# Kernel tuning notes

Measured on AMD Instinct MI355X. Metric: run time of the kernel, lower is better.

Reference implementation:

```python
import jax, jax.numpy as jnp
import numpy as np

B, H, K, T, OUT, NH = 512, 512, 6, 60, 2, 8

def _gelu(x):
    return jax.nn.gelu(x, approximate=False)  # torch nn.GELU default = exact erf

def _layernorm(x, g, b, eps=1e-5):
    m = jnp.mean(x, axis=-1, keepdims=True)
    v = jnp.var(x, axis=-1, keepdims=True)
    return (x - m) * jax.lax.rsqrt(v + eps) * g + b

def setup_inputs() -> dict:
    key = jax.random.key(0)
    ks = iter(jax.random.split(key, 40))
    def p(shape, scale=0.02):
        return jax.random.normal(next(ks), shape, dtype=jnp.float32) * scale
    return dict(
        interaction_ctx=p((B, H), 1.0),
        cooperative_ctx=p((B, H), 1.0),
        map_ctx=p((B, H), 1.0),
        mode_queries=p((K, H)),
        # context_proj: Linear(3H,H) -> GELU -> Linear(H,H)
        Wc1=p((3 * H, H)), bc1=jnp.zeros((H,), jnp.float32),
        Wc2=p((H, H)), bc2=jnp.zeros((H,), jnp.float32),
        # coarse_heads stacked over modes: Linear(H,2H)->GELU->Linear(2H,T*OUT)
        Wk1=p((K, H, 2 * H)), bk1=jnp.zeros((K, 2 * H), jnp.float32),
        Wk2=p((K, 2 * H, T * OUT)), bk2=jnp.zeros((K, T * OUT), jnp.float32),
        # traj_encoder: Linear(OUT,H)->GELU
        Wt=p((OUT, H)), bt=jnp.zeros((H,), jnp.float32),
        # refine_attn (MultiheadAttention) projections
        Wq_a=p((H, H)), bq_a=jnp.zeros((H,), jnp.float32),
        Wk_a=p((H, H)), bk_a=jnp.zeros((H,), jnp.float32),
        Wv_a=p((H, H)), bv_a=jnp.zeros((H,), jnp.float32),
        Wo_a=p((H, H)), bo_a=jnp.zeros((H,), jnp.float32),
        ln_g=jnp.ones((H,), jnp.float32), ln_b=jnp.zeros((H,), jnp.float32),
        # refine_heads stacked over modes: Linear(H,H)->GELU->Linear(H,OUT)
        Wr1=p((K, H, H)), br1=jnp.zeros((K, H), jnp.float32),
        Wr2=p((K, H, OUT)), br2=jnp.zeros((K, OUT), jnp.float32),
        # conf_head: Linear(H,64)->ReLU->Linear(64,1)
        Wf1=p((H, 64)), bf1=jnp.zeros((64,), jnp.float32),
        Wf2=p((64, 1)), bf2=jnp.zeros((1,), jnp.float32),
    )

def reference(interaction_ctx, cooperative_ctx, map_ctx, mode_queries,
              Wc1, bc1, Wc2, bc2, Wk1, bk1, Wk2, bk2, Wt, bt,
              Wq_a, bq_a, Wk_a, bk_a, Wv_a, bv_a, Wo_a, bo_a,
              ln_g, ln_b, Wr1, br1, Wr2, br2, Wf1, bf1, Wf2, bf2):
    # dropout layers are identity in eval mode
    combined = jnp.concatenate([interaction_ctx, cooperative_ctx, map_ctx], axis=-1)  # (B,3H)
    context = _gelu(combined @ Wc1 + bc1) @ Wc2 + bc2                                 # (B,H)
    mode_features = mode_queries[None, :, :] + context[:, None, :]                    # (B,K,H)

    # coarse heads: per-mode loop -> grouped GEMM over mode axis
    h = _gelu(jnp.einsum('bkh,khf->bkf', mode_features, Wk1) + bk1)                   # (B,K,2H)
    coarse = (jnp.einsum('bkf,kfo->bko', h, Wk2) + bk2).reshape(B, K, T, OUT)          # (B,K,T,OUT)

    traj_feats = _gelu(coarse @ Wt + bt)                                              # (B,K,T,H)

    # refine_attn: keys/values are context broadcast over T (all identical), so
    # softmax weights are exactly uniform and attention output == out_proj(v_ctx).
    # (grads through Wq_a/Wk_a are exactly zero for the same reason.)
    v = context @ Wv_a + bv_a                                                         # (B,H)
    attn_out = v @ Wo_a + bo_a                                                        # (B,H)

    refined_feats = _layernorm(traj_feats + attn_out[:, None, None, :], ln_g, ln_b)   # (B,K,T,H)

    # refine heads: grouped GEMM over mode axis
    r = _gelu(jnp.einsum('bkth,khf->bktf', refined_feats, Wr1) + br1[:, None, :])     # (B,K,T,H)
    offsets = jnp.einsum('bktf,kfo->bkto', r, Wr2) + br2[:, None, :]                  # (B,K,T,OUT)
    predictions = coarse + offsets

    conf = jax.nn.relu(mode_features @ Wf1 + bf1) @ Wf2 + bf2                         # (B,K,1)
    mode_probs = jax.nn.softmax(conf[..., 0], axis=-1)                                # (B,K)
    return predictions, mode_probs
```

## Files before the change

### kernel.cpp

```cpp
#include <hip/hip_runtime.h>
#include <math.h>

#define BB 512
#define HH 512
#define KK 6
#define TT 60
#define OO 2
#define H2 1024
#define TO 120
#define RFP 520
#define HSP 1032

typedef __bf16 bf16x8 __attribute__((ext_vector_type(8)));
typedef float  f32x4  __attribute__((ext_vector_type(4)));
typedef float  f32x16 __attribute__((ext_vector_type(16)));

__device__ __forceinline__ float bf2f(unsigned short u) {
    union { unsigned int i; float f; } v; v.i = ((unsigned int)u) << 16; return v.f;
}
__device__ __forceinline__ unsigned short f2bf(float f) {
    union { float f; unsigned int i; } v; v.f = f;
    unsigned int b = v.i;
    return (unsigned short)((b + 0x7FFFu + ((b >> 16) & 1u)) >> 16);
}
__device__ __forceinline__ unsigned int pack2bf(float a, float b) {
    union { __bf16 h[2]; unsigned int u; } v;
    v.h[0] = (__bf16)a; v.h[1] = (__bf16)b;
    return v.u;
}
__device__ __forceinline__ float gelu_exact(float x) {
    return 0.5f * x * (1.0f + erff(x * 0.70710678118654752f));
}

#if defined(__has_builtin)
#  if __has_builtin(__builtin_amdgcn_rcpf)
#    define FAST_RCP(x) __builtin_amdgcn_rcpf(x)
#  endif
#  if __has_builtin(__builtin_amdgcn_exp2f)
#    define FAST_EXP2(x) __builtin_amdgcn_exp2f(x)
#  endif
#endif
#ifndef FAST_RCP
#  define FAST_RCP(x) (1.0f / (x))
#endif
#ifndef FAST_EXP2
#  define FAST_EXP2(x) __expf((x) * 0.69314718056f)
#endif

__device__ __forceinline__ float gelu_cheap(float x) {
    float x2 = x * x;
    float z = x * fmaf(0.10294324f, x2, 2.3022082f);
    float e = FAST_EXP2(-z);
    return x * FAST_RCP(1.0f + e);
}

struct F8 { float v[8]; };
__device__ __forceinline__ F8 load8f(const float* p) {
    F8 r;
    float4 a = *(const float4*)p;
    float4 b = *(const float4*)(p + 4);
    r.v[0] = a.x; r.v[1] = a.y; r.v[2] = a.z; r.v[3] = a.w;
    r.v[4] = b.x; r.v[5] = b.y; r.v[6] = b.z; r.v[7] = b.w;
    return r;
}
__device__ __forceinline__ F8 load8b(const unsigned short* p) {
    ushort4 a = *(const ushort4*)p;
    ushort4 b = *(const ushort4*)(p + 4);
    F8 r;
    r.v[0] = bf2f(a.x); r.v[1] = bf2f(a.y); r.v[2] = bf2f(a.z); r.v[3] = bf2f(a.w);
    r.v[4] = bf2f(b.x); r.v[5] = bf2f(b.y); r.v[6] = bf2f(b.z); r.v[7] = bf2f(b.w);
    return r;
}

struct PKD { const float* src; unsigned short* dst; int F, N, NC, nch, steps, Z; };
struct PK8 { PKD e[8]; };

__global__ void k_pack(PK8 d) {
    int rid = blockIdx.x * 4 + (threadIdx.x >> 6);
    const int ln = threadIdx.x & 63;
    int i = 0;
    while (i < 7) {
        int tot = d.e[i].Z * d.e[i].nch * d.e[i].steps;
        if (rid < tot) break;
        rid -= tot; ++i;
    }
    const PKD e = d.e[i];
    const int per = e.nch * e.steps;
    const int z = rid / per;
    const int r = rid - z * per;
    const int nch = r / e.steps, step = r - nch * e.steps;
    const float* src = e.src + (size_t)z * e.F * e.N;
    unsigned short* dst = e.dst + ((size_t)z * per + r) * 512 + ln * 8;
    int f_base, n;
    if (e.NC == 16) { f_base = step * 32 + (ln >> 4) * 8; n = nch * 16 + (ln & 15); }
    else            { f_base = step * 16 + (ln >> 5) * 8; n = nch * 32 + (ln & 31); }
    if (n >= e.N) n = e.N - 1;
    unsigned int pk[4];
#pragma unroll
    for (int j = 0; j < 4; ++j) {
        unsigned short lo = f2bf(src[(size_t)(f_base + 2 * j) * e.N + n]);
        unsigned short hi = f2bf(src[(size_t)(f_base + 2 * j + 1) * e.N + n]);
        pk[j] = (unsigned int)lo | ((unsigned int)hi << 16);
    }
    *(uint4*)dst = make_uint4(pk[0], pk[1], pk[2], pk[3]);
}

template <bool CONCAT, bool GELU>
__launch_bounds__(256)
__global__ void k_gemm_m(const void* __restrict__ A0, const void* __restrict__ A1,
                         const void* __restrict__ A2, const unsigned short* __restrict__ BP,
                         const float* __restrict__ bias, unsigned short* __restrict__ C,
                         int Kd) {
    __shared__ __align__(16) unsigned short As[32 * RFP];
    const int tid = threadIdx.x;
    const int bm = blockIdx.x * 32;
    const int bn = blockIdx.y * 32;
    const int w = tid >> 6, ln = tid & 63;
    const int lane15 = ln & 15, quad = ln >> 4;
    const int mh = w >> 1;
    const int ng = w & 1;
    const int n = bn + ng * 16 + lane15;
    const int nchunks = Kd / HH;
    const int stepsTot = Kd / 32;
    const int nchB = blockIdx.y * 2 + ng;

    f32x4 acc0 = {0.f, 0.f, 0.f, 0.f};

    for (int kc = 0; kc < nchunks; ++kc) {
        {
            int r = tid >> 3, c0 = (tid & 7) * 64;
            unsigned short* dp = As + r * RFP + c0;
            if (CONCAT) {
                const float* src = (kc == 0) ? (const float*)A0
                                 : (kc == 1) ? (const float*)A1 : (const float*)A2;
                const float* sp = src + (bm + r) * HH + c0;
                for (int c = 0; c < 64; c += 8) {
                    F8 v = load8f(sp + c);
                    unsigned int pk[4];
#pragma unroll
                    for (int j = 0; j < 4; ++j)
                        pk[j] = pack2bf(v.v[2 * j], v.v[2 * j + 1]);
                    *(uint4*)(dp + c) = make_uint4(pk[0], pk[1], pk[2], pk[3]);
                }
            } else {
                const unsigned short* sp = (const unsigned short*)A0 + (bm + r) * HH + c0;
                for (int c = 0; c < 64; c += 8)
                    *(uint4*)(dp + c) = *(const uint4*)(sp + c);
            }
        }
        __syncthreads();
        const unsigned short* bp = BP + ((size_t)nchB * stepsTot + kc * 16) * 512 + ln * 8;
#pragma unroll
        for (int f0 = 0; f0 < HH; f0 += 32) {
            bf16x8 a0 = *(const bf16x8*)(As + (mh * 16 + lane15) * RFP + f0 + quad * 8);
            bf16x8 bf = *(const bf16x8*)(bp);
            bp += 512;
            acc0 = __builtin_amdgcn_mfma_f32_16x16x32_bf16(a0, bf, acc0, 0, 0, 0);
        }
        __syncthreads();
    }
    const float bb = bias[n];
#pragma unroll
    for (int reg = 0; reg < 4; ++reg) {
        float v0 = acc0[reg] + bb;
        if (GELU) v0 = gelu_exact(v0);
        C[(bm + mh * 16 + quad * 4 + reg) * HH + n] = f2bf(v0);
    }
}

__launch_bounds__(256)
__global__ void k_g1w(const float* __restrict__ I0, const float* __restrict__ I1,
                      const float* __restrict__ I2, const unsigned short* __restrict__ Wc1P,
                      const float* __restrict__ bc1, unsigned short* __restrict__ tmp,
                      const float* __restrict__ Wv, const unsigned short* __restrict__ WoP,
                      const float* __restrict__ WoF, const float* __restrict__ bv,
                      const float* __restrict__ bo,
                      unsigned short* __restrict__ wvop, float* __restrict__ bvo)
{
    __shared__ __align__(16) unsigned short As[32 * RFP];
    const int tid = threadIdx.x;
    const int w = tid >> 6, ln = tid & 63;
    const int lane15 = ln & 15, quad = ln >> 4;
    const int mh = w >> 1, ng = w & 1;

    if (blockIdx.x >= 256) {
        const int gbid = blockIdx.x - 256;
        const int bm = (gbid & 15) * 32;
        const int bn = (gbid >> 4) * 32;
        {
            int r = tid >> 3, c0 = (tid & 7) * 64;
            const float* sp = Wv + (size_t)(bm + r) * HH + c0;
            unsigned short* dp = As + r * RFP + c0;
            for (int c = 0; c < 64; c += 8) {
                F8 v = load8f(sp + c);
                unsigned int pk[4];
#pragma unroll
                for (int j = 0; j < 4; ++j)
                    pk[j] = pack2bf(v.v[2 * j], v.v[2 * j + 1]);
                *(uint4*)(dp + c) = make_uint4(pk[0], pk[1], pk[2], pk[3]);
            }
        }
        __syncthreads();
        const int n = bn + ng * 16 + lane15;
        const int nchB = (bn >> 4) + ng;
        f32x4 acc0 = {0.f, 0.f, 0.f, 0.f};
        const unsigned short* bp = WoP + (size_t)nchB * 16 * 512 + ln * 8;
#pragma unroll
        for (int f0 = 0; f0 < HH; f0 += 32) {
            bf16x8 a0 = *(const bf16x8*)(As + (mh * 16 + lane15) * RFP + f0 + quad * 8);
            bf16x8 bf = *(const bf16x8*)(bp);
            bp += 512;
            acc0 = __builtin_amdgcn_mfma_f32_16x16x32_bf16(a0, bf, acc0, 0, 0, 0);
        }
        const int step2 = bm >> 5;
        const int nch2 = n >> 4;
#pragma unroll
        for (int reg = 0; reg < 4; ++reg) {
            const int r5 = mh * 16 + quad * 4 + reg;
            const int ln2 = ((r5 >> 3) << 4) | lane15;
            wvop[((size_t)(nch2 * 16 + step2)) * 512 + ln2 * 8 + (r5 & 7)] = f2bf(acc0[reg]);
        }
        if (bm == 0 && w == 0 && ln < 32) {
            const int nn = bn + ln;
            float s = 0.f;
            for (int f = 0; f < HH; ++f) s = fmaf(bv[f], WoF[(size_t)f * HH + nn], s);
            bvo[nn] = s + bo[nn];
        }
        return;
    }

    const int bm = (blockIdx.x & 15) * 32;
    const int by = blockIdx.x >> 4;
    const int bn = by * 32;
    const int n = bn + ng * 16 + lane15;
    const int nchB = by * 2 + ng;
    const int stepsTot = 48;

    f32x4 acc0 = {0.f, 0.f, 0.f, 0.f};

    for (int kc = 0; kc < 3; ++kc) {
        {
            int r = tid >> 3, c0 = (tid & 7) * 64;
            unsigned short* dp = As + r * RFP + c0;
            const float* src = (kc == 0) ? I0 : (kc == 1) ? I1 : I2;
            const float* sp = src + (size_t)(bm + r) * HH + c0;
            for (int c = 0; c < 64; c += 8) {
                F8 v = load8f(sp + c);
                unsigned int pk[4];
#pragma unroll
                for (int j = 0; j < 4; ++j)
                    pk[j] = pack2bf(v.v[2 * j], v.v[2 * j + 1]);
                *(uint4*)(dp + c) = make_uint4(pk[0], pk[1], pk[2], pk[3]);
            }
        }
        __syncthreads();
        const unsigned short* bp = Wc1P + ((size_t)nchB * stepsTot + kc * 16) * 512 + ln * 8;
#pragma unroll
        for (int f0 = 0; f0 < HH; f0 += 32) {
            bf16x8 a0 = *(const bf16x8*)(As + (mh * 16 + lane15) * RFP + f0 + quad * 8);
            bf16x8 bf = *(const bf16x8*)(bp);
            bp += 512;
            acc0 = __builtin_amdgcn_mfma_f32_16x16x32_bf16(a0, bf, acc0, 0, 0, 0);
        }
        __syncthreads();
    }
    const float bb = bc1[n];
#pragma unroll
    for (int reg = 0; reg < 4; ++reg)
        tmp[(bm + mh * 16 + quad * 4 + reg) * HH + n] = f2bf(gelu_exact(acc0[reg] + bb));
}

__launch_bounds__(512)
__global__ void k_bcg(const unsigned short* __restrict__ ctx, const float* __restrict__ mq,
                      const unsigned short* __restrict__ Wk1P, const float* __restrict__ bk1,
                      const unsigned short* __restrict__ Wk2P, const float* __restrict__ bk2,
                      const unsigned short* __restrict__ Wf1P, const float* __restrict__ bf1,
                      const float* __restrict__ Wf2, const float* __restrict__ bf2v,
                      unsigned short* __restrict__ coarse_out, float* __restrict__ conf_out,
                      const unsigned short* __restrict__ WvoP, const float* __restrict__ bvo,
                      unsigned short* __restrict__ attn_out)
{
    __shared__ __align__(16) unsigned short shbuf[24832];

    const int tid = threadIdx.x;
    const int w = tid >> 6;
    const int ln = tid & 63;
    const int lane15 = ln & 15;
    const int quad = ln >> 4;

    if (blockIdx.x >= 192) {
        unsigned short* As = shbuf;
        const int gbid = blockIdx.x - 192;
        const int bm = (gbid & 15) * 32;
        const int gy = gbid >> 4;
        const int bn = gy * 64;
        const int mh = w >> 2;
        const int ng = w & 3;
        const int n = bn + ng * 16 + lane15;
        const int nchB = gy * 4 + ng;

        {
            int r = tid >> 4, c0 = (tid & 15) * 32;
            const unsigned short* sp = ctx + (bm + r) * HH + c0;
            unsigned short* dp = As + r * RFP + c0;
            for (int c = 0; c < 32; c += 8)
                *(uint4*)(dp + c) = *(const uint4*)(sp + c);
        }
        __syncthreads();
        f32x4 acc0 = {0.f, 0.f, 0.f, 0.f};
        const unsigned short* bp = WvoP + (size_t)nchB * 16 * 512 + ln * 8;
#pragma unroll
        for (int f0 = 0; f0 < HH; f0 += 32) {
            bf16x8 a0 = *(const bf16x8*)(As + (mh * 16 + lane15) * RFP + f0 + quad * 8);
            bf16x8 bf = *(const bf16x8*)(bp);
            bp += 512;
            acc0 = __builtin_amdgcn_mfma_f32_16x16x32_bf16(a0, bf, acc0, 0, 0, 0);
        }
        const float bb = bvo[n];
#pragma unroll
        for (int reg = 0; reg < 4; ++reg)
            attn_out[(bm + mh * 16 + quad * 4 + reg) * HH + n] = f2bf(acc0[reg] + bb);
        return;
    }

    unsigned short* mf = shbuf;
    unsigned short* hs = shbuf + 16 * RFP;
    const int k = blockIdx.x % KK;
    const int b0 = (blockIdx.x / KK) * 16;

    {
        int r = tid >> 5;
        int c0 = (tid & 31) * 16;
        const unsigned short* cp = ctx + (b0 + r) * HH + c0;
        const float* qp = mq + k * HH + c0;
        unsigned short* dp = mf + r * RFP + c0;
        for (int c = 0; c < 16; c += 8) {
            F8 cv = load8b(cp + c);
            F8 qv = load8f(qp + c);
            unsigned int pk[4];
#pragma unroll
            for (int j = 0; j < 4; ++j)
                pk[j] = pack2bf(cv.v[2 * j] + qv.v[2 * j], cv.v[2 * j + 1] + qv.v[2 * j + 1]);
            *(uint4*)(dp + c) = make_uint4(pk[0], pk[1], pk[2], pk[3]);
        }
    }
    __syncthreads();

    {
        const unsigned short* wk1p = Wk1P + (size_t)k * (64 * 16 * 512);
        const float* bk1p = bk1 + k * H2;
        for (int g = 0; g < 8; ++g) {
            const int n = w * 128 + g * 16 + lane15;
            f32x4 acc0 = {0.f,0.f,0.f,0.f};
            const unsigned short* bp = wk1p + (size_t)((w * 8 + g) * 16) * 512 + ln * 8;
#pragma unroll
            for (int f0 = 0; f0 < HH; f0 += 32) {
                bf16x8 a0 = *(const bf16x8*)(mf + lane15 * RFP + f0 + quad * 8);
                bf16x8 bf = *(const bf16x8*)(bp);
                bp += 512;
                acc0 = __builtin_amdgcn_mfma_f32_16x16x32_bf16(a0, bf, acc0, 0, 0, 0);
            }
            const float bias = bk1p[n];
#pragma unroll
            for (int reg = 0; reg < 4; ++reg)
                hs[(quad * 4 + reg) * HSP + n] = f2bf(gelu_exact(acc0[reg] + bias));
        }
    }
    __syncthreads();

    {
        const unsigned short* wk2p = Wk2P + (size_t)k * (8 * 32 * 512);
        const int n = w * 16 + lane15;
        f32x4 acc0 = {0.f,0.f,0.f,0.f};
        const unsigned short* bp = wk2p + (size_t)(w * 32) * 512 + ln * 8;
#pragma unroll
        for (int f0 = 0; f0 < H2; f0 += 32) {
            bf16x8 a0 = *(const bf16x8*)(hs + lane15 * HSP + f0 + quad * 8);
            bf16x8 bf = *(const bf16x8*)(bp);
            bp += 512;
            acc0 = __builtin_amdgcn_mfma_f32_16x16x32_bf16(a0, bf, acc0, 0, 0, 0);
        }
        if (n < TO) {
            const float bias = bk2[k * TO + n];
#pragma unroll
            for (int reg = 0; reg < 4; ++reg)
                coarse_out[((b0 + quad * 4 + reg) * KK + k) * TO + n] = f2bf(acc0[reg] + bias);
        }
    }

    if (w == 0) {
        f32x4 acc[4];
#pragma unroll
        for (int nt = 0; nt < 4; ++nt) { f32x4 z = {0.f,0.f,0.f,0.f}; acc[nt] = z; }
#pragma unroll
        for (int f0 = 0; f0 < HH; f0 += 32) {
            const int step = f0 >> 5;
            bf16x8 a0 = *(const bf16x8*)(mf + lane15 * RFP + f0 + quad * 8);
#pragma unroll
            for (int nt = 0; nt < 4; ++nt) {
                bf16x8 bf = *(const bf16x8*)(Wf1P + (size_t)(nt * 16 + step) * 512 + ln * 8);
                acc[nt] = __builtin_amdgcn_mfma_f32_16x16x32_bf16(a0, bf, acc[nt], 0, 0, 0);
            }
        }
        const float b2 = bf2v[0];
#pragma unroll
        for (int reg = 0; reg < 4; ++reg) {
            float s = 0.f;
#pragma unroll
            for (int nt = 0; nt < 4; ++nt) {
                const int n = nt * 16 + lane15;
                s = fmaf(fmaxf(acc[nt][reg] + bf1[n], 0.f), Wf2[n], s);
            }
#pragma unroll
            for (int off = 1; off < 16; off <<= 1) s += __shfl_xor(s, off);
            if (lane15 == 0)
                conf_out[(b0 + quad * 4 + reg) * KK + k] = s + b2;
        }
    }
}

__launch_bounds__(512, 4)
__global__ void k_ef(
    const unsigned short* __restrict__ attn, const unsigned short* __restrict__ coarse_ws,
    const float* __restrict__ Wt,  const float* __restrict__ bt,
    const float* __restrict__ lng, const float* __restrict__ lnb,
    const unsigned short* __restrict__ Wr1P, const float* __restrict__ br1,
    const float* __restrict__ Wr2, const float* __restrict__ br2,
    float* __restrict__ pred_out,
    const float* __restrict__ conf, float* __restrict__ probs)
{
    __shared__ __align__(16) unsigned short rf[64 * RFP];
    __shared__ float coarse[TO];
    __shared__ float br1s[HH];
    __shared__ float2 wr2s[HH];
    __shared__ float po2[8][64][2];

    const int tid = threadIdx.x;
    const int b = blockIdx.x / KK;
    const int k = blockIdx.x % KK;
    const int w = tid >> 6;
    const int ln = tid & 63;
    const int lane31 = ln & 31;
    const int hf = ln >> 5;
    const int cbase = ln * 8;

    const unsigned short* attb = attn + b * HH;

    if (tid < TO) coarse[tid] = bf2f(coarse_ws[(b * KK + k) * TO + tid]);
    br1s[tid] = br1[k * HH + tid];
    wr2s[tid] = ((const float2*)Wr2)[(size_t)k * HH + tid];

    if (k == 0 && tid == 448) {
        float v[KK]; float m = -1e30f;
#pragma unroll
        for (int i = 0; i < KK; ++i) { v[i] = conf[b * KK + i]; m = fmaxf(m, v[i]); }
        float s = 0.f;
#pragma unroll
        for (int i = 0; i < KK; ++i) { v[i] = __expf(v[i] - m); s += v[i]; }
        float inv = 1.0f / s;
#pragma unroll
        for (int i = 0; i < KK; ++i) probs[b * KK + i] = v[i] * inv;
    }
    __syncthreads();

    {
        F8 w0 = load8f(Wt + cbase);
        F8 w1 = load8f(Wt + HH + cbase);
        F8 b8 = load8f(bt + cbase);
        F8 g8 = load8f(lng + cbase);
        F8 bb8 = load8f(lnb + cbase);
        F8 a8 = load8b(attb + cbase);
#pragma unroll
        for (int g = 0; g < 2; ++g) {
            float x[4][8];
            float s[4], s2[4];
#pragma unroll
            for (int r = 0; r < 4; ++r) {
                const int t = w + 8 * (g * 4 + r);
                float ss = 0.f, ss2 = 0.f;
                if (t < 60) {
                    const float co0 = coarse[2 * t], co1 = coarse[2 * t + 1];
#pragma unroll
                    for (int j = 0; j < 8; ++j) {
                        float vv = fmaf(co0, w0.v[j], fmaf(co1, w1.v[j], b8.v[j]));
                        vv = gelu_cheap(vv) + a8.v[j];
                        x[r][j] = vv; ss += vv; ss2 = fmaf(vv, vv, ss2);
                    }
                } else {
#pragma unroll
                    for (int j = 0; j < 8; ++j) x[r][j] = 0.f;
                }
                s[r] = ss; s2[r] = ss2;
            }
#pragma unroll
            for (int off = 32; off > 0; off >>= 1) {
#pragma unroll
                for (int r = 0; r < 4; ++r) {
                    s[r] += __shfl_xor(s[r], off);
                    s2[r] += __shfl_xor(s2[r], off);
                }
            }
#pragma unroll
            for (int r = 0; r < 4; ++r) {
                const int t = w + 8 * (g * 4 + r);
                if (t < 60) {
                    float mean = s[r] * (1.0f / HH);
                    float var = fmaf(-mean, mean, s2[r] * (1.0f / HH));
                    float inv = rsqrtf(var + 1e-5f);
                    unsigned int pk[4];
#pragma unroll
                    for (int j = 0; j < 4; ++j) {
                        float y0 = fmaf((x[r][2 * j] - mean) * inv, g8.v[2 * j], bb8.v[2 * j]);
                        float y1 = fmaf((x[r][2 * j + 1] - mean) * inv, g8.v[2 * j + 1], bb8.v[2 * j + 1]);
                        pk[j] = pack2bf(y0, y1);
                    }
                    *(uint4*)(rf + t * RFP + cbase) = make_uint4(pk[0], pk[1], pk[2], pk[3]);
                } else {
                    *(uint4*)(rf + t * RFP + cbase) = make_uint4(0, 0, 0, 0);
                }
            }
        }
    }
    __syncthreads();

    {
        const unsigned short* bp0 = Wr1P + (size_t)k * (16 * 32 * 512)
                                  + (size_t)(w * 2) * 32 * 512 + ln * 8;
        const unsigned short* bp1 = bp0 + 32 * 512;
        const int n0 = w * 64;
        const unsigned short* a0p = rf + lane31 * RFP + hf * 8;
        const unsigned short* a1p = a0p + 32 * RFP;

        f32x16 acc00 = {0.f,0.f,0.f,0.f,0.f,0.f,0.f,0.f,0.f,0.f,0.f,0.f,0.f,0.f,0.f,0.f};
        f32x16 acc01 = acc00, acc10 = acc00, acc11 = acc00;

        __builtin_amdgcn_s_setprio(1);
#pragma unroll
        for (int st = 0; st < 32; ++st) {
            const int k0 = st * 16;
            bf16x8 A0 = *(const bf16x8*)(a0p + k0);
            bf16x8 A1 = *(const bf16x8*)(a1p + k0);
            bf16x8 B0 = *(const bf16x8*)(bp0 + st * 512);
            bf16x8 B1 = *(const bf16x8*)(bp1 + st * 512);
            acc00 = __builtin_amdgcn_mfma_f32_32x32x16_bf16(B0, A0, acc00, 0, 0, 0);
            acc01 = __builtin_amdgcn_mfma_f32_32x32x16_bf16(B1, A0, acc01, 0, 0, 0);
            acc10 = __builtin_amdgcn_mfma_f32_32x32x16_bf16(B0, A1, acc10, 0, 0, 0);
            acc11 = __builtin_amdgcn_mfma_f32_32x32x16_bf16(B1, A1, acc11, 0, 0, 0);
        }
        __builtin_amdgcn_s_setprio(0);

        float p00 = 0.f, p01 = 0.f, p10 = 0.f, p11 = 0.f;
#pragma unroll
        for (int nt = 0; nt < 2; ++nt) {
#pragma unroll
            for (int reg = 0; reg < 16; ++reg) {
                const int n = n0 + nt * 32 + (reg & 3) + 8 * (reg >> 2) + 4 * hf;
                const float bb = br1s[n];
                const float2 w2 = wr2s[n];
                const float a0v = nt ? acc01[reg] : acc00[reg];
                const float a1v = nt ? acc11[reg] : acc10[reg];
                const float rv0 = gelu_cheap(a0v + bb);
                const float rv1 = gelu_cheap(a1v + bb);
                p00 = fmaf(rv0, w2.x, p00);
                p01 = fmaf(rv0, w2.y, p01);
                p10 = fmaf(rv1, w2.x, p10);
                p11 = fmaf(rv1, w2.y, p11);
            }
        }
        p00 += __shfl_xor(p00, 32);
        p01 += __shfl_xor(p01, 32);
        p10 += __shfl_xor(p10, 32);
        p11 += __shfl_xor(p11, 32);
        if (ln < 32) {
            *(float2*)&po2[w][lane31][0]      = make_float2(p00, p01);
            *(float2*)&po2[w][32 + lane31][0] = make_float2(p10, p11);
        }
    }
    __syncthreads();

    if (tid < TO) {
        int t = tid >> 1, o = tid & 1;
        float s = 0.f;
#pragma unroll
        for (int ww = 0; ww < 8; ++ww) s += po2[ww][t][o];
        pred_out[((b * KK + k) * TT + t) * 2 + o] = coarse[tid] + s + br2[k * 2 + o];
    }
}

extern "C" void kernel_launch(void* const* d_in, const int* in_sizes, int n_in,
                              void* d_out, int out_size, void* d_ws, size_t ws_size,
                              hipStream_t stream) {
    const float* I0  = (const float*)d_in[0];
    const float* I1  = (const float*)d_in[1];
    const float* I2  = (const float*)d_in[2];
    const float* MQ  = (const float*)d_in[3];
    const float* Wc1 = (const float*)d_in[4];
    const float* bc1 = (const float*)d_in[5];
    const float* Wc2 = (const float*)d_in[6];
    const float* bc2 = (const float*)d_in[7];
    const float* Wk1 = (const float*)d_in[8];
    const float* bk1 = (const float*)d_in[9];
    const float* Wk2 = (const float*)d_in[10];
    const float* bk2 = (const float*)d_in[11];
    const float* Wt  = (const float*)d_in[12];
    const float* bt  = (const float*)d_in[13];
    const float* Wv  = (const float*)d_in[18];
    const float* bv  = (const float*)d_in[19];
    const float* Wo  = (const float*)d_in[20];
    const float* bo  = (const float*)d_in[21];
    const float* lng = (const float*)d_in[22];
    const float* lnb = (const float*)d_in[23];
    const float* Wr1 = (const float*)d_in[24];
    const float* br1 = (const float*)d_in[25];
    const float* Wr2 = (const float*)d_in[26];
    const float* br2 = (const float*)d_in[27];
    const float* Wf1 = (const float*)d_in[28];
    const float* bf1 = (const float*)d_in[29];
    const float* Wf2 = (const float*)d_in[30];
    const float* bf2v = (const float*)d_in[31];

    unsigned short* wsu   = (unsigned short*)d_ws;
    unsigned short* wc1p  = wsu;
    unsigned short* wc2p  = wsu + 786432;
    unsigned short* wvop  = wsu + 1048576;
    unsigned short* wop   = wsu + 1310720;
    unsigned short* wk1p  = wsu + 1572864;
    unsigned short* wk2p  = wsu + 4718592;
    unsigned short* wf1p  = wsu + 5505024;
    unsigned short* wr1p  = wsu + 5537792;
    unsigned short* ctx   = wsu + 7110656;
    unsigned short* attn  = wsu + 7372800;
    unsigned short* tmp   = wsu + 7634944;
    unsigned short* coarse= wsu + 7897088;
    float* conf = (float*)(wsu + 8265728);
    float* bvo  = (float*)(wsu + 8271872);

    float* pred = (float*)d_out;
    float* probs = pred + BB * KK * TT * OO;

    PK8 pk;
    pk.e[0] = {Wc1, wc1p, 3 * HH, HH, 16, 32, 48, 1};
    pk.e[1] = {Wc2, wc2p, HH, HH, 16, 32, 16, 1};
    pk.e[2] = {Wc2, wc2p, HH, HH, 16, 0, 16, 1};
    pk.e[3] = {Wo,  wop,  HH, HH, 16, 32, 16, 1};
    pk.e[4] = {Wk1, wk1p, HH, H2, 16, 64, 16, KK};
    pk.e[5] = {Wk2, wk2p, H2, TO, 16, 8, 32, KK};
    pk.e[6] = {Wf1, wf1p, HH, 64, 16, 4, 16, 1};
    pk.e[7] = {Wr1, wr1p, HH, HH, 32, 16, 32, KK};
    k_pack<<<dim3(3344), 256, 0, stream>>>(pk);

    k_g1w<<<dim3(512), 256, 0, stream>>>(I0, I1, I2, wc1p, bc1, tmp,
                                         Wv, wop, Wo, bv, bo, wvop, bvo);

    k_gemm_m<false, false><<<dim3(16, 16), 256, 0, stream>>>(tmp, nullptr, nullptr, wc2p, bc2, ctx, HH);

    k_bcg<<<dim3(320), 512, 0, stream>>>(ctx, MQ, wk1p, bk1, wk2p, bk2, wf1p, bf1, Wf2, bf2v,
                                         coarse, conf, wvop, bvo, attn);

    k_ef<<<dim3(BB * KK), 512, 0, stream>>>(attn, coarse, Wt, bt, lng, lnb,
                                            wr1p, br1, Wr2, br2, pred, conf, probs);
}
```

Before: 322.4 us.

## Split weight packing and overlap later packs with first GEMM kernel

The single packing kernel is split. Only the weights needed by the first GEMM kernel (Wc1, Wo) are packed up front. The remaining packs (Wc2, Wk1, Wk2, Wf1, Wr1) run as extra blocks appended to the k_g1w launch, so that work overlaps with the first GEMM instead of serialising before it. The refine kernel also reads coarse values directly from global memory and drops a block barrier. This trades a shorter critical path for a larger, mixed-role grid, and relies on the remaining syncs still covering the shared-memory loads of br1s and wr2s.

After: 380.8 us, median of 2. +18.1%, slower.

```diff
diff --git a/kernel.cpp b/kernel.cpp
--- a/kernel.cpp
+++ b/kernel.cpp
@@ -75,9 +75,7 @@
 struct PKD { const float* src; unsigned short* dst; int F, N, NC, nch, steps, Z; };
 struct PK8 { PKD e[8]; };
 
-__global__ void k_pack(PK8 d) {
-    int rid = blockIdx.x * 4 + (threadIdx.x >> 6);
-    const int ln = threadIdx.x & 63;
+__device__ __forceinline__ void pack_one(const PK8& d, int rid, int ln) {
     int i = 0;
     while (i < 7) {
         int tot = d.e[i].Z * d.e[i].nch * d.e[i].steps;
@@ -103,6 +101,10 @@
         pk[j] = (unsigned int)lo | ((unsigned int)hi << 16);
     }
     *(uint4*)dst = make_uint4(pk[0], pk[1], pk[2], pk[3]);
+}
+
+__global__ void k_pack(PK8 d) {
+    pack_one(d, blockIdx.x * 4 + (threadIdx.x >> 6), threadIdx.x & 63);
 }
 
 template <bool CONCAT, bool GELU>
@@ -175,13 +177,19 @@
                       const float* __restrict__ Wv, const unsigned short* __restrict__ WoP,
                       const float* __restrict__ WoF, const float* __restrict__ bv,
                       const float* __restrict__ bo,
-                      unsigned short* __restrict__ wvop, float* __restrict__ bvo)
+                      unsigned short* __restrict__ wvop, float* __restrict__ bvo,
+                      PK8 pkb)
 {
     __shared__ __align__(16) unsigned short As[32 * RFP];
     const int tid = threadIdx.x;
     const int w = tid >> 6, ln = tid & 63;
     const int lane15 = ln & 15, quad = ln >> 4;
     const int mh = w >> 1, ng = w & 1;
+
+    if (blockIdx.x >= 512) {
+        pack_one(pkb, (blockIdx.x - 512) * 4 + w, ln);
+        return;
+    }
 
     if (blockIdx.x >= 256) {
         const int gbid = blockIdx.x - 256;
@@ -445,8 +453,9 @@
     const int cbase = ln * 8;
 
     const unsigned short* attb = attn + b * HH;
-
-    if (tid < TO) coarse[tid] = bf2f(coarse_ws[(b * KK + k) * TO + tid]);
+    const unsigned short* cw = coarse_ws + (b * KK + k) * TO;
+
+    if (tid < TO) coarse[tid] = bf2f(cw[tid]);
     br1s[tid] = br1[k * HH + tid];
     wr2s[tid] = ((const float2*)Wr2)[(size_t)k * HH + tid];
 
@@ -461,7 +470,6 @@
 #pragma unroll
         for (int i = 0; i < KK; ++i) probs[b * KK + i] = v[i] * inv;
     }
-    __syncthreads();
 
     {
         F8 w0 = load8f(Wt + cbase);
@@ -479,7 +487,9 @@
                 const int t = w + 8 * (g * 4 + r);
                 float ss = 0.f, ss2 = 0.f;
                 if (t < 60) {
-                    const float co0 = coarse[2 * t], co1 = coarse[2 * t + 1];
+                    unsigned int cc = *(const unsigned int*)(cw + 2 * t);
+                    const float co0 = bf2f((unsigned short)(cc & 0xffffu));
+                    const float co1 = bf2f((unsigned short)(cc >> 16));
 #pragma unroll
                     for (int j = 0; j < 8; ++j) {
                         float vv = fmaf(co0, w0.v[j], fmaf(co1, w1.v[j], b8.v[j]));
@@ -638,19 +648,25 @@
     float* pred = (float*)d_out;
     float* probs = pred + BB * KK * TT * OO;
 
-    PK8 pk;
-    pk.e[0] = {Wc1, wc1p, 3 * HH, HH, 16, 32, 48, 1};
-    pk.e[1] = {Wc2, wc2p, HH, HH, 16, 32, 16, 1};
-    pk.e[2] = {Wc2, wc2p, HH, HH, 16, 0, 16, 1};
-    pk.e[3] = {Wo,  wop,  HH, HH, 16, 32, 16, 1};
-    pk.e[4] = {Wk1, wk1p, HH, H2, 16, 64, 16, KK};
-    pk.e[5] = {Wk2, wk2p, H2, TO, 16, 8, 32, KK};
-    pk.e[6] = {Wf1, wf1p, HH, 64, 16, 4, 16, 1};
-    pk.e[7] = {Wr1, wr1p, HH, HH, 32, 16, 32, KK};
-    k_pack<<<dim3(3344), 256, 0, stream>>>(pk);
-
-    k_g1w<<<dim3(512), 256, 0, stream>>>(I0, I1, I2, wc1p, bc1, tmp,
-                                         Wv, wop, Wo, bv, bo, wvop, bvo);
+    PK8 pkA;
+    pkA.e[0] = {Wc1, wc1p, 3 * HH, HH, 16, 32, 48, 1};
+    pkA.e[1] = {Wo,  wop,  HH, HH, 16, 32, 16, 1};
+    pkA.e[2] = {Wc2, wc2p, HH, HH, 16, 0, 16, 1};
+    pkA.e[3] = pkA.e[2]; pkA.e[4] = pkA.e[2]; pkA.e[5] = pkA.e[2];
+    pkA.e[6] = pkA.e[2]; pkA.e[7] = pkA.e[2];
+    k_pack<<<dim3(512), 256, 0, stream>>>(pkA);
+
+    PK8 pkB;
+    pkB.e[0] = {Wc2, wc2p, HH, HH, 16, 32, 16, 1};
+    pkB.e[1] = {Wk1, wk1p, HH, H2, 16, 64, 16, KK};
+    pkB.e[2] = {Wk2, wk2p, H2, TO, 16, 8, 32, KK};
+    pkB.e[3] = {Wf1, wf1p, HH, 64, 16, 4, 16, 1};
+    pkB.e[4] = {Wr1, wr1p, HH, HH, 32, 16, 32, KK};
+    pkB.e[5] = {Wc2, wc2p, HH, HH, 16, 0, 16, 1};
+    pkB.e[6] = pkB.e[5]; pkB.e[7] = pkB.e[5];
+
+    k_g1w<<<dim3(3344), 256, 0, stream>>>(I0, I1, I2, wc1p, bc1, tmp,
+                                          Wv, wop, Wo, bv, bo, wvop, bvo, pkB);
 
     k_gemm_m<false, false><<<dim3(16, 16), 256, 0, stream>>>(tmp, nullptr, nullptr, wc2p, bc2, ctx, HH);
 
```
